# Optimization experiments

Hardware: AMD Instinct MI355X
Metric: run time of the kernel (lower is better)

The kernel has to match this reference:

```python
import jax, jax.numpy as jnp
import numpy as np

B, L, D_MODEL = 2, 2048, 1024
D_STATE, D_CONV, EXPAND, DT_RANK = 16, 4, 2, 64
D_INNER = EXPAND * D_MODEL


def setup_inputs() -> dict:
    key = jax.random.key(0)
    ks = jax.random.split(key, 12)
    s = 0.02
    A_log = jnp.log(jnp.broadcast_to(jnp.arange(1, D_STATE + 1, dtype=jnp.float32), (D_INNER, D_STATE)))
    return {
        "x": jax.random.normal(ks[0], (B, L, D_MODEL), jnp.float32),
        "W_in": jax.random.normal(ks[1], (2 * D_INNER, D_MODEL), jnp.float32) * s,
        "conv_w": jax.random.normal(ks[2], (D_INNER, 1, D_CONV), jnp.float32) * 0.2,
        "conv_b": jax.random.normal(ks[3], (D_INNER,), jnp.float32) * s,
        "W_xp": jax.random.normal(ks[4], (DT_RANK + 2 * D_STATE, D_INNER), jnp.float32) * s,
        "W_dt": jax.random.normal(ks[5], (D_INNER, DT_RANK), jnp.float32) * 0.1,
        "b_dt": jax.random.uniform(ks[6], (D_INNER,), jnp.float32, -4.6, -2.3),  # ~softplus^-1 of small dt
        "A_log": A_log,
        "D": jnp.ones((D_INNER,), jnp.float32),
        "W_out_ssm": jax.random.normal(ks[7], (D_MODEL, D_INNER), jnp.float32) * s,
        "W_out": jax.random.normal(ks[8], (D_MODEL, D_MODEL), jnp.float32) * s,
        "b_out": jnp.zeros((D_MODEL,), jnp.float32),
    }


def _mamba_block(x, W_in, conv_w, conv_b, W_xp, W_dt, b_dt, A_log, D, W_out_ssm, W_out, b_out):
    d_inner = conv_b.shape[0]
    d_state = A_log.shape[1]
    dt_rank = W_dt.shape[1]
    d_conv = conv_w.shape[-1]

    # in_proj -> x branch and gate z
    xz = x @ W_in.T                         # [B, L, 2*d_inner]
    xin, z = jnp.split(xz, 2, axis=-1)

    # causal depthwise conv over time
    xc = jnp.transpose(xin, (0, 2, 1))      # [B, d_inner, L]
    xc = jax.lax.conv_general_dilated(
        xc, conv_w, window_strides=(1,), padding=[(d_conv - 1, 0)],
        feature_group_count=d_inner)
    xc = jax.nn.silu(xc + conv_b[None, :, None])
    xs = jnp.transpose(xc, (0, 2, 1))       # [B, L, d_inner]

    # input-dependent dt, B, C
    x_dbl = xs @ W_xp.T                     # [B, L, dt_rank + 2*d_state]
    dt, Bm, Cm = jnp.split(x_dbl, [dt_rank, dt_rank + d_state], axis=-1)
    dt = jax.nn.softplus(dt @ W_dt.T + b_dt)  # [B, L, d_inner]

    A = -jnp.exp(A_log)                     # [d_inner, d_state]

    def step(h, inp):
        dt_t, B_t, C_t, x_t = inp           # [B,di] [B,ds] [B,ds] [B,di]
        dA = jnp.exp(dt_t[:, :, None] * A)                      # [B, di, ds]
        h = h * dA + (dt_t * x_t)[:, :, None] * B_t[:, None, :]  # [B, di, ds]
        y = jnp.einsum('bds,bs->bd', h, C_t)
        return h, y

    h0 = jnp.zeros((x.shape[0], d_inner, d_state), x.dtype)
    tm = lambda a: jnp.swapaxes(a, 0, 1)    # time-major
    _, ys = jax.lax.scan(step, h0, (tm(dt), tm(Bm), tm(Cm), tm(xs)))
    y = jnp.swapaxes(ys, 0, 1)              # [B, L, d_inner]

    y = y + xs * D
    y = y * jax.nn.silu(z)
    y = y @ W_out_ssm.T                     # mamba-internal out_proj -> d_model
    return y @ W_out.T + b_out              # wrapper out_proj


def reference(x, W_in, conv_w, conv_b, W_xp, W_dt, b_dt, A_log, D, W_out_ssm, W_out, b_out):
    return _mamba_block(x, W_in, conv_w, conv_b, W_xp, W_dt, b_dt, A_log, D, W_out_ssm, W_out, b_out)
```

## Files before the change

kernel.cpp:

```cpp
#include <hip/hip_runtime.h>
#include <hip/hip_bf16.h>
#include <cmath>
#include <cstdint>

typedef __bf16 bf16_t;
typedef bf16_t bf16x8 __attribute__((ext_vector_type(8)));
typedef bf16_t bf16x4 __attribute__((ext_vector_type(4)));
typedef float f32x4 __attribute__((ext_vector_type(4)));

#define BB 2
#define LL 2048
#define DMODEL 1024
#define DINNER 2048
#define DSTATE 16
#define NC 64
#define CHUNK 32
#define KSEG 256

#define EXP2F(x) __builtin_amdgcn_exp2f(x)

#define CVT_N0 1048576
#define CVT_N1 2097152
#define CVT_N2 2129920
#define CVT_N3 2392064
#define CVT_NB0 9344
#define CVT_NB1 10368
#define CVT_NBT 10880
__global__ __launch_bounds__(256) void k_cvt_all(
    const float* __restrict__ x, const float* __restrict__ Win,
    const float* __restrict__ Wdt, const float* __restrict__ Wo,
    const float* __restrict__ Wxp, const float* __restrict__ Wos,
    bf16_t* __restrict__ x_b, bf16_t* __restrict__ Win_b,
    bf16_t* __restrict__ Wdt_b, bf16_t* __restrict__ Wo_b,
    bf16_t* __restrict__ Wxp_b, bf16_t* __restrict__ WosT_b) {
    const int tid = threadIdx.x;
    if (blockIdx.x < CVT_NB0) {
        int i = blockIdx.x * 256 + tid;
        const float* src; bf16_t* dst; int j;
        if (i < CVT_N0)      { src = x;   dst = x_b;   j = i; }
        else if (i < CVT_N1) { src = Win; dst = Win_b; j = i - CVT_N0; }
        else if (i < CVT_N2) { src = Wdt; dst = Wdt_b; j = i - CVT_N1; }
        else                 { src = Wo;  dst = Wo_b;  j = i - CVT_N2; }
        float4 v = reinterpret_cast<const float4*>(src)[j];
        bf16x4 o;
        o[0] = (bf16_t)v.x; o[1] = (bf16_t)v.y; o[2] = (bf16_t)v.z; o[3] = (bf16_t)v.w;
        reinterpret_cast<bf16x4*>(dst)[j] = o;
    } else if (blockIdx.x < CVT_NB1) {
        int i = (blockIdx.x - CVT_NB0) * 256 + tid;
        int r = i >> 11, c = i & (DINNER - 1);
        float v = (r < 96) ? Wxp[r * DINNER + c] : 0.f;
        Wxp_b[i] = (bf16_t)v;
    } else {
        __shared__ float tile[64][65];
        const int bid = blockIdx.x - CVT_NB1;
        const int m0 = (bid & 15) * 64;
        const int d0 = (bid >> 4) * 64;
        const int dl = tid & 63;
        #pragma unroll 4
        for (int i = 0; i < 16; ++i) {
            const int mr = (tid >> 6) + i * 4;
            tile[dl][mr] = Wos[(size_t)(m0 + mr) * DINNER + d0 + dl];
        }
        __syncthreads();
        const int dr = tid >> 2;
        const int q  = tid & 3;
        bf16_t* op = WosT_b + (size_t)(d0 + dr) * DMODEL + m0 + q * 16;
        bf16x8 v0, v1;
        #pragma unroll
        for (int j = 0; j < 8; ++j) v0[j] = (bf16_t)tile[dr][q * 16 + j];
        #pragma unroll
        for (int j = 0; j < 8; ++j) v1[j] = (bf16_t)tile[dr][q * 16 + 8 + j];
        reinterpret_cast<bf16x8*>(op)[0] = v0;
        reinterpret_cast<bf16x8*>(op)[1] = v1;
    }
}

__device__ __forceinline__ void gload16(const void* g, void* l) {
    __builtin_amdgcn_global_load_lds(
        (const __attribute__((address_space(1))) void*)g,
        (__attribute__((address_space(3))) void*)l,
        16, 0, 0);
}

__global__ __launch_bounds__(512) void k_gemm256(
    const bf16_t* __restrict__ x_b, const bf16_t* __restrict__ Win_b,
    bf16_t* __restrict__ xin_b, bf16_t* __restrict__ zsT) {
    __shared__ bf16_t lds[65536];
    const int tid = threadIdx.x;
    const int wid = tid >> 6, lane = tid & 63;

    const int bid = (blockIdx.x & 7) * 32 + (blockIdx.x >> 3);
    const bf16_t* A; const bf16_t* Bt; int m0, n0, sub;
    if (bid < 128) {
        sub = 0; A = x_b; Bt = Win_b;
        m0 = (bid >> 3) * 256; n0 = (bid & 7) * 256;
    } else {
        sub = 1; A = Win_b + (size_t)DINNER * DMODEL; Bt = x_b;
        const int t2 = bid - 128;
        m0 = (t2 >> 4) * 256; n0 = (t2 & 15) * 256;
    }
    const int wr = wid >> 2, wc = wid & 3;
    f32x4 acc[8][4] = {};

    const int srow = tid >> 3;
    const int k8p = (tid & 7) ^ (srow & 7);
    const bf16_t* apA = A + (size_t)(m0 + srow) * 1024 + k8p * 8;
    const bf16_t* apB = Bt + (size_t)(n0 + srow) * 1024 + k8p * 8;

    auto stageA = [&](int slot, int kt) {
        char* b0 = (char*)lds + slot * 32768 + wid * 1024;
        const bf16_t* src = apA + kt * 64;
        gload16(src, b0);
        gload16(src + (size_t)64 * 1024, b0 + 8192);
        gload16(src + (size_t)128 * 1024, b0 + 16384);
        gload16(src + (size_t)192 * 1024, b0 + 24576);
    };
    auto stageB = [&](int slot, int kt) {
        char* b0 = (char*)lds + 65536 + slot * 32768 + wid * 1024;
        const bf16_t* src = apB + kt * 64;
        gload16(src, b0);
        gload16(src + (size_t)64 * 1024, b0 + 8192);
        gload16(src + (size_t)128 * 1024, b0 + 16384);
        gload16(src + (size_t)192 * 1024, b0 + 24576);
    };

    const int lm = lane & 15, lq = lane >> 4;

    const bf16_t* pA0[8]; const bf16_t* pA1[8];
    const bf16_t* pB0[4]; const bf16_t* pB1[4];
    #pragma unroll
    for (int i = 0; i < 8; ++i) {
        const int rr = lm + i * 16;
        const int e0 = wr * 8192 + rr * 64 + (lq ^ (rr & 7)) * 8;
        pA0[i] = lds + e0;
        pA1[i] = lds + (e0 ^ 32);
    }
    #pragma unroll
    for (int j = 0; j < 4; ++j) {
        const int rr = (wc & 1) * 64 + lm + j * 16;
        const int e0 = 32768 + (wc >> 1) * 8192 + rr * 64 + (lq ^ (rr & 7)) * 8;
        pB0[j] = lds + e0;
        pB1[j] = lds + (e0 ^ 32);
    }

    auto body = [&](int t, int s) {
        asm volatile("s_waitcnt vmcnt(0)" ::: "memory");
        __builtin_amdgcn_sched_barrier(0);
        __builtin_amdgcn_s_barrier();
        __builtin_amdgcn_sched_barrier(0);
        if (t + 1 < 16) {
            stageA(s ^ 1, t + 1);
            stageB(s ^ 1, t + 1);
        }
        {
            bf16x8 fa[8], fb[4];
            #pragma unroll
            for (int i = 0; i < 8; ++i) fa[i] = *(const bf16x8*)(pA0[i] + s * 16384);
            #pragma unroll
            for (int j = 0; j < 4; ++j) fb[j] = *(const bf16x8*)(pB0[j] + s * 16384);
            __builtin_amdgcn_s_setprio(1);
            #pragma unroll
            for (int i = 0; i < 8; ++i)
                #pragma unroll
                for (int j = 0; j < 4; ++j)
                    acc[i][j] = __builtin_amdgcn_mfma_f32_16x16x32_bf16(fa[i], fb[j], acc[i][j], 0, 0, 0);
            __builtin_amdgcn_s_setprio(0);
        }
        {
            bf16x8 fa[8], fb[4];
            #pragma unroll
            for (int i = 0; i < 8; ++i) fa[i] = *(const bf16x8*)(pA1[i] + s * 16384);
            #pragma unroll
            for (int j = 0; j < 4; ++j) fb[j] = *(const bf16x8*)(pB1[j] + s * 16384);
            __builtin_amdgcn_s_setprio(1);
            #pragma unroll
            for (int i = 0; i < 8; ++i)
                #pragma unroll
                for (int j = 0; j < 4; ++j)
                    acc[i][j] = __builtin_amdgcn_mfma_f32_16x16x32_bf16(fa[i], fb[j], acc[i][j], 0, 0, 0);
            __builtin_amdgcn_s_setprio(0);
        }
    };

    stageA(0, 0);
    stageB(0, 0);
    for (int tt = 0; tt < 8; ++tt) {
        body(2 * tt, 0);
        body(2 * tt + 1, 1);
    }

    const int row0 = m0 + wr * 128 + lq * 4;
    const int col0 = n0 + wc * 64 + lm;
    #pragma unroll
    for (int i = 0; i < 8; ++i) {
        #pragma unroll
        for (int j = 0; j < 4; ++j) {
            #pragma unroll
            for (int r = 0; r < 4; ++r) {
                const int row = row0 + i * 16 + r;
                const int c = col0 + j * 16;
                float v = acc[i][j][r];
                if (sub == 0) xin_b[(size_t)row * DINNER + c] = (bf16_t)v;
                else          zsT[(size_t)row * (BB * LL) + c] = (bf16_t)(v / (1.f + __expf(-v)));
            }
        }
    }
}

enum { EPI_BF16 = 0, EPI_BIAS = 1, EPI_SOFTPLUS_RB = 3, EPI_PARTK = 4 };

template <int EPI>
__global__ __launch_bounds__(512) void k_gemm_bt(
    const bf16_t* __restrict__ A, const bf16_t* __restrict__ Bt,
    int M, int N, int Kloop, int lda, int ldb,
    float* __restrict__ C, bf16_t* __restrict__ Cb,
    const float* __restrict__ bias,
    float* __restrict__ o_part) {
    __shared__ bf16_t sA[2][128 * 32];
    __shared__ bf16_t sB[2][128 * 32];
    const int tid = threadIdx.x;
    const int wid = tid >> 6, lane = tid & 63;
    const int bx = (blockIdx.x & 7) * ((int)gridDim.x >> 3) + (blockIdx.x >> 3);
    int m0, n0, k0 = 0, seg = 0;
    if (EPI == EPI_PARTK) {
        m0 = (bx & 31) << 7;
        n0 = 0;
        seg = bx >> 5;
        k0 = seg * KSEG;
    } else {
        const int ntile = N >> 7;
        m0 = (bx / ntile) << 7;
        n0 = (bx % ntile) << 7;
    }
    const int wr = wid >> 2, wc = wid & 3;
    f32x4 acc[4][2] = {};

    const bf16_t* ap = A + (size_t)(m0 + (tid >> 2)) * lda + (tid & 3) * 8 + k0;
    const bf16_t* bp = Bt + (size_t)(n0 + (tid >> 2)) * ldb + (tid & 3) * 8 + k0;
    const int lm = lane & 15, lk = (lane >> 4) * 8;

    auto stage = [&](int buf, int kt) {
        char* dA = (char*)sA[buf] + wid * 1024;
        char* dB = (char*)sB[buf] + wid * 1024;
        gload16(ap + kt, dA);
        gload16(bp + kt, dB);
    };

    stage(0, 0);
    __syncthreads();
    int cur = 0;
    for (int kt = 0; kt < Kloop; kt += 32) {
        if (kt + 32 < Kloop) stage(cur ^ 1, kt + 32);
        const bf16_t* rA = sA[cur] + (wr * 64 + lm) * 32 + lk;
        const bf16_t* rB = sB[cur] + (wc * 32 + lm) * 32 + lk;
        bf16x8 fa[4], fb[2];
        #pragma unroll
        for (int i = 0; i < 4; ++i) fa[i] = *(const bf16x8*)(rA + i * 16 * 32);
        #pragma unroll
        for (int j = 0; j < 2; ++j) fb[j] = *(const bf16x8*)(rB + j * 16 * 32);
        __builtin_amdgcn_s_setprio(1);
        #pragma unroll
        for (int i = 0; i < 4; ++i)
            #pragma unroll
            for (int j = 0; j < 2; ++j)
                acc[i][j] = __builtin_amdgcn_mfma_f32_16x16x32_bf16(fa[i], fb[j], acc[i][j], 0, 0, 0);
        __builtin_amdgcn_s_setprio(0);
        __syncthreads();
        cur ^= 1;
    }

    const int row0 = m0 + wr * 64 + (lane >> 4) * 4;
    const int col0 = n0 + wc * 32 + lm;
    float* Cp = (EPI == EPI_PARTK)
        ? o_part + (size_t)seg * ((size_t)4096 * 128)
        : C;
    #pragma unroll
    for (int i = 0; i < 4; ++i) {
        #pragma unroll
        for (int j = 0; j < 2; ++j) {
            #pragma unroll
            for (int r = 0; r < 4; ++r) {
                int row = row0 + i * 16 + r;
                int c = col0 + j * 16;
                float v = acc[i][j][r];
                if (EPI == EPI_BF16) {
                    Cb[(size_t)row * N + c] = (bf16_t)v;
                } else if (EPI == EPI_BIAS) {
                    C[(size_t)row * N + c] = v + bias[c];
                } else if (EPI == EPI_SOFTPLUS_RB) {
                    float xv = v + bias[row];
                    float sp = fmaxf(xv, 0.f) + log1pf(__expf(-fabsf(xv)));
                    Cb[(size_t)row * N + c] = (bf16_t)sp;
                } else {
                    Cp[(size_t)row * 128 + c] = v;
                }
            }
        }
    }
}

__global__ __launch_bounds__(256) void k_split_reduce(
    const float* __restrict__ part, bf16_t* __restrict__ dtr,
    float* __restrict__ Bmf, float* __restrict__ Cmf) {
    int idx = blockIdx.x * 256 + threadIdx.x;
    int row = idx >> 7, c = idx & 127;
    float s = 0.f;
    #pragma unroll
    for (int g = 0; g < 8; ++g) s += part[(size_t)g * (4096 * 128) + idx];
    if (c < 64) dtr[(size_t)row * 64 + c] = (bf16_t)s;
    else if (c < 80) Bmf[(size_t)row * 16 + (c - 64)] = s;
    else if (c < 96) Cmf[(size_t)row * 16 + (c - 80)] = s;
}

__global__ __launch_bounds__(256) void k_conv(
    const bf16_t* __restrict__ xin, const float* __restrict__ cw,
    const float* __restrict__ cb, bf16_t* __restrict__ xs_b,
    bf16_t* __restrict__ xsT) {
    __shared__ float tile[64][65];
    const int tid = threadIdx.x;
    const int d0  = (blockIdx.x & 31) * 64;
    const int bl0 = (blockIdx.x >> 5) * 64;
    const int dl = tid & 63;
    const int d  = d0 + dl;
    const float w0 = cw[d * 4], w1 = cw[d * 4 + 1], w2 = cw[d * 4 + 2], w3 = cw[d * 4 + 3];
    const float bias = cb[d];
    const int l0 = bl0 & (LL - 1);
    #pragma unroll 4
    for (int i = 0; i < 16; ++i) {
        const int blr = (tid >> 6) + i * 4;
        const int bl = bl0 + blr;
        const int l  = l0 + blr;
        const bf16_t* rp = xin + (size_t)bl * DINNER + d;
        float acc = fmaf(w3, (float)rp[0], bias);
        if (l >= 1) acc = fmaf(w2, (float)rp[-(int)DINNER], acc);
        if (l >= 2) acc = fmaf(w1, (float)rp[-2 * (int)DINNER], acc);
        if (l >= 3) acc = fmaf(w0, (float)rp[-3 * (int)DINNER], acc);
        float sv = acc / (1.f + __expf(-acc));
        xs_b[(size_t)bl * DINNER + d] = (bf16_t)sv;
        tile[dl][blr] = sv;
    }
    __syncthreads();
    const int dr = tid >> 2;
    const int q  = tid & 3;
    bf16_t* op = xsT + (size_t)(d0 + dr) * (BB * LL) + bl0 + q * 16;
    bf16x8 v0, v1;
    #pragma unroll
    for (int j = 0; j < 8; ++j) v0[j] = (bf16_t)tile[dr][q * 16 + j];
    #pragma unroll
    for (int j = 0; j < 8; ++j) v1[j] = (bf16_t)tile[dr][q * 16 + 8 + j];
    reinterpret_cast<bf16x8*>(op)[0] = v0;
    reinterpret_cast<bf16x8*>(op)[1] = v1;
}


__global__ __launch_bounds__(256) void k_scan_p1(
    const bf16_t* __restrict__ dtT, const bf16_t* __restrict__ xsT,
    const float* __restrict__ Bm, const float* __restrict__ A_log,
    float* __restrict__ alpha, float* __restrict__ beta) {
    __shared__ float sB[CHUNK * 16];
    const int db = blockIdx.x & 7;
    const int ck = (blockIdx.x >> 3) & (NC - 1);
    const int b  = blockIdx.x >> 9;
    const int tid = threadIdx.x;
    const int d  = db * 256 + tid;
    const int t0 = ck * CHUNK;

    const float* Bsrc = Bm + ((size_t)b * LL + t0) * 16;
    sB[tid] = Bsrc[tid];
    sB[tid + 256] = Bsrc[tid + 256];

    f32x4 a2[4];
    #pragma unroll
    for (int q = 0; q < 4; ++q) {
        f32x4 av = reinterpret_cast<const f32x4*>(A_log + d * 16)[q];
        #pragma unroll
        for (int j = 0; j < 4; ++j) a2[q][j] = -__expf(av[j]) * 1.44269504f;
    }
    const bf16x8* dtp = reinterpret_cast<const bf16x8*>(dtT + (size_t)d * (BB * LL) + b * LL + t0);
    const bf16x8* xsp = reinterpret_cast<const bf16x8*>(xsT + (size_t)d * (BB * LL) + b * LL + t0);

    bf16x8 dtl[4], xsl[4];
    #pragma unroll
    for (int q = 0; q < 4; ++q) dtl[q] = dtp[q];
    #pragma unroll
    for (int q = 0; q < 4; ++q) xsl[q] = xsp[q];

    __syncthreads();

    float al[16], be[16];
    #pragma unroll
    for (int s = 0; s < 16; ++s) { al[s] = 1.f; be[s] = 0.f; }

    #pragma unroll
    for (int t = 0; t < CHUNK; ++t) {
        float dtv = (float)dtl[t >> 3][t & 7];
        float xv  = (float)xsl[t >> 3][t & 7];
        float dtx = dtv * xv;
        #pragma unroll
        for (int q = 0; q < 4; ++q) {
            f32x4 Bq = *reinterpret_cast<const f32x4*>(sB + t * 16 + q * 4);
            #pragma unroll
            for (int j = 0; j < 4; ++j) {
                const int s = q * 4 + j;
                float dA = EXP2F(dtv * a2[q][j]);
                al[s] *= dA;
                be[s] = fmaf(be[s], dA, dtx * Bq[j]);
            }
        }
    }
    float* ap = alpha + ((size_t)(b * NC + ck)) * (DINNER * 16) + (size_t)d * 16;
    float* bp = beta  + ((size_t)(b * NC + ck)) * (DINNER * 16) + (size_t)d * 16;
    #pragma unroll
    for (int q = 0; q < 4; ++q) {
        f32x4 av, bv;
        #pragma unroll
        for (int j = 0; j < 4; ++j) { av[j] = al[q * 4 + j]; bv[j] = be[q * 4 + j]; }
        reinterpret_cast<f32x4*>(ap)[q] = av;
        reinterpret_cast<f32x4*>(bp)[q] = bv;
    }
}

__global__ __launch_bounds__(256) void k_scan_p2(
    const float* __restrict__ alpha, const float* __restrict__ beta,
    float* __restrict__ H) {
    const int gid = blockIdx.x * 256 + threadIdx.x;
    const int b = gid >> 15, r = gid & 32767;
    float h = 0.f;
    #pragma unroll 8
    for (int ck = 0; ck < NC; ++ck) {
        const size_t i = ((size_t)(b * NC + ck)) * 32768 + r;
        H[i] = h;
        h = fmaf(alpha[i], h, beta[i]);
    }
}

__global__ __launch_bounds__(256) void k_scan_p3(
    const bf16_t* __restrict__ dtT, const bf16_t* __restrict__ xsT,
    const float* __restrict__ Bm, const float* __restrict__ Cm,
    const bf16_t* __restrict__ zsT, const float* __restrict__ A_log,
    const float* __restrict__ Dp, const float* __restrict__ H,
    bf16_t* __restrict__ y) {
    __shared__ float sB[CHUNK * 16];
    __shared__ float sC[CHUNK * 16];
    const int db = blockIdx.x & 7;
    const int ck = (blockIdx.x >> 3) & (NC - 1);
    const int b  = blockIdx.x >> 9;
    const int tid = threadIdx.x;
    const int d  = db * 256 + tid;
    const int t0 = ck * CHUNK;

    const float* Bsrc = Bm + ((size_t)b * LL + t0) * 16;
    const float* Csrc = Cm + ((size_t)b * LL + t0) * 16;
    sB[tid] = Bsrc[tid];
    sB[tid + 256] = Bsrc[tid + 256];
    sC[tid] = Csrc[tid];
    sC[tid + 256] = Csrc[tid + 256];

    f32x4 a2[4];
    #pragma unroll
    for (int q = 0; q < 4; ++q) {
        f32x4 av = reinterpret_cast<const f32x4*>(A_log + d * 16)[q];
        #pragma unroll
        for (int j = 0; j < 4; ++j) a2[q][j] = -__expf(av[j]) * 1.44269504f;
    }
    const float Dd = Dp[d];
    const bf16x8* dtp = reinterpret_cast<const bf16x8*>(dtT + (size_t)d * (BB * LL) + b * LL + t0);
    const bf16x8* xsp = reinterpret_cast<const bf16x8*>(xsT + (size_t)d * (BB * LL) + b * LL + t0);
    const bf16x8* zp  = reinterpret_cast<const bf16x8*>(zsT + (size_t)d * (BB * LL) + b * LL + t0);
    bf16_t* yp = y + ((size_t)b * LL + t0) * DINNER + d;

    bf16x8 dtl[4], xsl[4], zsl[4];
    #pragma unroll
    for (int q = 0; q < 4; ++q) dtl[q] = dtp[q];
    #pragma unroll
    for (int q = 0; q < 4; ++q) xsl[q] = xsp[q];
    #pragma unroll
    for (int q = 0; q < 4; ++q) zsl[q] = zp[q];

    float h[16];
    {
        const f32x4* hp = reinterpret_cast<const f32x4*>(H + ((size_t)(b * NC + ck)) * 32768 + (size_t)d * 16);
        #pragma unroll
        for (int q = 0; q < 4; ++q) {
            f32x4 hv = hp[q];
            #pragma unroll
            for (int j = 0; j < 4; ++j) h[q * 4 + j] = hv[j];
        }
    }

    __syncthreads();

    #pragma unroll
    for (int t = 0; t < CHUNK; ++t) {
        float dtv = (float)dtl[t >> 3][t & 7];
        float xv  = (float)xsl[t >> 3][t & 7];
        float zv  = (float)zsl[t >> 3][t & 7];
        float dtx = dtv * xv;
        float yacc = 0.f;
        #pragma unroll
        for (int q = 0; q < 4; ++q) {
            f32x4 Bq = *reinterpret_cast<const f32x4*>(sB + t * 16 + q * 4);
            f32x4 Cq = *reinterpret_cast<const f32x4*>(sC + t * 16 + q * 4);
            #pragma unroll
            for (int j = 0; j < 4; ++j) {
                const int s = q * 4 + j;
                float dA = EXP2F(dtv * a2[q][j]);
                h[s] = fmaf(h[s], dA, dtx * Bq[j]);
                yacc = fmaf(h[s], Cq[j], yacc);
            }
        }
        float yv = (yacc + xv * Dd) * zv;
        yp[(size_t)t * DINNER] = (bf16_t)yv;
    }
}

extern "C" void kernel_launch(void* const* d_in, const int* in_sizes, int n_in,
                              void* d_out, int out_size, void* d_ws, size_t ws_size,
                              hipStream_t stream) {
    const float* x      = (const float*)d_in[0];
    const float* W_in   = (const float*)d_in[1];
    const float* conv_w = (const float*)d_in[2];
    const float* conv_b = (const float*)d_in[3];
    const float* W_xp   = (const float*)d_in[4];
    const float* W_dt   = (const float*)d_in[5];
    const float* b_dt   = (const float*)d_in[6];
    const float* A_log  = (const float*)d_in[7];
    const float* Dvec   = (const float*)d_in[8];
    const float* W_os   = (const float*)d_in[9];
    const float* W_o    = (const float*)d_in[10];
    const float* b_o    = (const float*)d_in[11];
    float* out = (float*)d_out;

    char* base = (char*)d_ws;
    size_t off = 0;
    auto alloc = [&](size_t bytes) -> char* {
        char* p = base + off;
        off += (bytes + 255) & ~(size_t)255;
        return p;
    };
    const int MR = BB * LL;
    bf16_t* x_b   = (bf16_t*)alloc((size_t)MR * DMODEL * 2);
    bf16_t* Win_b = (bf16_t*)alloc((size_t)4096 * 1024 * 2);
    bf16_t* xin_b = (bf16_t*)alloc((size_t)MR * DINNER * 2);
    bf16_t* xs_b  = (bf16_t*)alloc((size_t)MR * DINNER * 2);
    bf16_t* zsT   = (bf16_t*)alloc((size_t)DINNER * MR * 2);
    bf16_t* xsT   = (bf16_t*)alloc((size_t)DINNER * MR * 2);
    bf16_t* dtT_b = (bf16_t*)alloc((size_t)DINNER * MR * 2);
    float*  Hbuf  = (float*)alloc((size_t)BB * NC * DINNER * 16 * 4);
    bf16_t* y_b   = (bf16_t*)alloc((size_t)MR * DINNER * 2);
    bf16_t* dtr_b = (bf16_t*)alloc((size_t)MR * 64 * 2);
    float*  Bmf   = (float*)alloc((size_t)MR * 16 * 4);
    float*  Cmf   = (float*)alloc((size_t)MR * 16 * 4);
    bf16_t* Wxp_b = (bf16_t*)alloc((size_t)128 * DINNER * 2);
    bf16_t* Wdt_b = (bf16_t*)alloc((size_t)DINNER * 64 * 2);
    bf16_t* WosT_b= (bf16_t*)alloc((size_t)DINNER * DMODEL * 2);
    bf16_t* Wo_b  = (bf16_t*)alloc((size_t)DMODEL * DMODEL * 2);
    bf16_t* Wc_b  = (bf16_t*)alloc((size_t)DMODEL * DINNER * 2);

    float* alphab = (float*)xin_b;
    float* betab  = (float*)x_b;
    float* partk  = Hbuf;

    k_cvt_all<<<CVT_NBT, 256, 0, stream>>>(
        x, W_in, W_dt, W_o, W_xp, W_os,
        x_b, Win_b, Wdt_b, Wo_b, Wxp_b, WosT_b);

    k_gemm_bt<EPI_BF16><<<(DMODEL / 128) * (DINNER / 128), 512, 0, stream>>>(
        Wo_b, WosT_b, DMODEL, DINNER, DMODEL, DMODEL, DMODEL,
        nullptr, Wc_b, nullptr, nullptr);
    k_gemm256<<<256, 512, 0, stream>>>(x_b, Win_b, xin_b, zsT);
    k_conv<<<(MR / 64) * (DINNER / 64), 256, 0, stream>>>(xin_b, conv_w, conv_b, xs_b, xsT);
    k_gemm_bt<EPI_PARTK><<<8 * 32, 512, 0, stream>>>(
        xs_b, Wxp_b, MR, 128, KSEG, DINNER, DINNER,
        nullptr, nullptr, nullptr, partk);
    k_split_reduce<<<(MR * 128) / 256, 256, 0, stream>>>(partk, dtr_b, Bmf, Cmf);
    k_gemm_bt<EPI_SOFTPLUS_RB><<<(DINNER / 128) * (MR / 128), 512, 0, stream>>>(
        Wdt_b, dtr_b, DINNER, MR, 64, 64, 64,
        nullptr, dtT_b, b_dt, nullptr);
    k_scan_p1<<<BB * NC * (DINNER / 256), 256, 0, stream>>>(dtT_b, xsT, Bmf, A_log, alphab, betab);
    k_scan_p2<<<(BB * DINNER * DSTATE) / 256, 256, 0, stream>>>(alphab, betab, Hbuf);
    k_scan_p3<<<BB * NC * (DINNER / 256), 256, 0, stream>>>(dtT_b, xsT, Bmf, Cmf, zsT, A_log, Dvec, Hbuf, y_b);
    k_gemm_bt<EPI_BIAS><<<(MR / 128) * (DMODEL / 128), 512, 0, stream>>>(
        y_b, Wc_b, MR, DMODEL, DINNER, DINNER, DINNER,
        out, nullptr, b_o, nullptr);
}
```

Measured before the change: 240.5 us.

## Add async-LDS 128x128 GEMM for weight fold/out-proj and store scan state in bf16

Adds a new 128x128-tile bf16 GEMM kernel that uses direct global-to-LDS loads (gload16), XOR-swizzled LDS, K=64 double buffering and s_setprio around the MFMA blocks. It replaces the older GEMM for the W_out·W_out_ssm weight fold and for the final output projection, aiming to cut load latency and LDS bank conflicts. Separately, the chunked-scan intermediates (alpha, beta, chunk-start H) are now stored in bf16 instead of fp32, halving their memory traffic. The bf16 state carries accuracy risk, because errors in the recurrence can accumulate across chunks.

```diff
diff --git a/kernel.cpp b/kernel.cpp
--- a/kernel.cpp
+++ b/kernel.cpp
@@ -210,6 +210,123 @@
 enum { EPI_BF16 = 0, EPI_BIAS = 1, EPI_SOFTPLUS_RB = 3, EPI_PARTK = 4 };
 
 template <int EPI>
+__global__ __launch_bounds__(512) void k_gemm_cd128(
+    const bf16_t* __restrict__ A, const bf16_t* __restrict__ Bt,
+    int N, int Ktiles, int lda, int ldb,
+    float* __restrict__ C, bf16_t* __restrict__ Cb,
+    const float* __restrict__ bias) {
+    __shared__ bf16_t lds[32768];
+    const int tid = threadIdx.x;
+    const int wid = tid >> 6, lane = tid & 63;
+    const int bx = (blockIdx.x & 7) * ((int)gridDim.x >> 3) + (blockIdx.x >> 3);
+    const int ntile = N >> 7;
+    const int m0 = (bx / ntile) << 7;
+    const int n0 = (bx % ntile) << 7;
+    const int wr = wid >> 2, wc = wid & 3;
+    f32x4 acc[4][2] = {};
+
+    const int srow = tid >> 3;
+    const int k8p = (tid & 7) ^ (srow & 7);
+    const bf16_t* apA = A + (size_t)(m0 + srow) * lda + k8p * 8;
+    const bf16_t* apB = Bt + (size_t)(n0 + srow) * ldb + k8p * 8;
+
+    auto stageA = [&](int slot, int kt) {
+        char* b0 = (char*)lds + slot * 16384 + wid * 1024;
+        const bf16_t* src = apA + kt * 64;
+        gload16(src, b0);
+        gload16(src + (size_t)64 * lda, b0 + 8192);
+    };
+    auto stageB = [&](int slot, int kt) {
+        char* b0 = (char*)lds + 32768 + slot * 16384 + wid * 1024;
+        const bf16_t* src = apB + kt * 64;
+        gload16(src, b0);
+        gload16(src + (size_t)64 * ldb, b0 + 8192);
+    };
+
+    const int lm = lane & 15, lq = lane >> 4;
+
+    const bf16_t* pA0[4]; const bf16_t* pA1[4];
+    const bf16_t* pB0[2]; const bf16_t* pB1[2];
+    #pragma unroll
+    for (int i = 0; i < 4; ++i) {
+        const int rr = lm + i * 16;
+        const int e0 = wr * 4096 + rr * 64 + (lq ^ (rr & 7)) * 8;
+        pA0[i] = lds + e0;
+        pA1[i] = lds + (e0 ^ 32);
+    }
+    #pragma unroll
+    for (int j = 0; j < 2; ++j) {
+        const int rr = wc * 32 + lm + j * 16;
+        const int e0 = 16384 + rr * 64 + (lq ^ (rr & 7)) * 8;
+        pB0[j] = lds + e0;
+        pB1[j] = lds + (e0 ^ 32);
+    }
+
+    auto body = [&](int t, int s) {
+        asm volatile("s_waitcnt vmcnt(0)" ::: "memory");
+        __builtin_amdgcn_sched_barrier(0);
+        __builtin_amdgcn_s_barrier();
+        __builtin_amdgcn_sched_barrier(0);
+        if (t + 1 < Ktiles) {
+            stageA(s ^ 1, t + 1);
+            stageB(s ^ 1, t + 1);
+        }
+        {
+            bf16x8 fa[4], fb[2];
+            #pragma unroll
+            for (int i = 0; i < 4; ++i) fa[i] = *(const bf16x8*)(pA0[i] + s * 8192);
+            #pragma unroll
+            for (int j = 0; j < 2; ++j) fb[j] = *(const bf16x8*)(pB0[j] + s * 8192);
+            __builtin_amdgcn_s_setprio(1);
+            #pragma unroll
+            for (int i = 0; i < 4; ++i)
+                #pragma unroll
+                for (int j = 0; j < 2; ++j)
+                    acc[i][j] = __builtin_amdgcn_mfma_f32_16x16x32_bf16(fa[i], fb[j], acc[i][j], 0, 0, 0);
+            __builtin_amdgcn_s_setprio(0);
+        }
+        {
+            bf16x8 fa[4], fb[2];
+            #pragma unroll
+            for (int i = 0; i < 4; ++i) fa[i] = *(const bf16x8*)(pA1[i] + s * 8192);
+            #pragma unroll
+            for (int j = 0; j < 2; ++j) fb[j] = *(const bf16x8*)(pB1[j] + s * 8192);
+            __builtin_amdgcn_s_setprio(1);
+            #pragma unroll
+            for (int i = 0; i < 4; ++i)
+                #pragma unroll
+                for (int j = 0; j < 2; ++j)
+                    acc[i][j] = __builtin_amdgcn_mfma_f32_16x16x32_bf16(fa[i], fb[j], acc[i][j], 0, 0, 0);
+            __builtin_amdgcn_s_setprio(0);
+        }
+    };
+
+    stageA(0, 0);
+    stageB(0, 0);
+    for (int tt = 0; tt < (Ktiles >> 1); ++tt) {
+        body(2 * tt, 0);
+        body(2 * tt + 1, 1);
+    }
+
+    const int row0 = m0 + wr * 64 + lq * 4;
+    const int col0 = n0 + wc * 32 + lm;
+    #pragma unroll
+    for (int i = 0; i < 4; ++i) {
+        #pragma unroll
+        for (int j = 0; j < 2; ++j) {
+            #pragma unroll
+            for (int r = 0; r < 4; ++r) {
+                const int row = row0 + i * 16 + r;
+                const int c = col0 + j * 16;
+                float v = acc[i][j][r];
+                if (EPI == EPI_BF16) Cb[(size_t)row * N + c] = (bf16_t)v;
+                else                 C[(size_t)row * N + c] = v + bias[c];
+            }
+        }
+    }
+}
+
+template <int EPI>
 __global__ __launch_bounds__(512) void k_gemm_bt(
     const bf16_t* __restrict__ A, const bf16_t* __restrict__ Bt,
     int M, int N, int Kloop, int lda, int ldb,
@@ -283,11 +400,7 @@
                 int row = row0 + i * 16 + r;
                 int c = col0 + j * 16;
                 float v = acc[i][j][r];
-                if (EPI == EPI_BF16) {
-                    Cb[(size_t)row * N + c] = (bf16_t)v;
-                } else if (EPI == EPI_BIAS) {
-                    C[(size_t)row * N + c] = v + bias[c];
-                } else if (EPI == EPI_SOFTPLUS_RB) {
+                if (EPI == EPI_SOFTPLUS_RB) {
                     float xv = v + bias[row];
                     float sp = fmaxf(xv, 0.f) + log1pf(__expf(-fabsf(xv)));
                     Cb[(size_t)row * N + c] = (bf16_t)sp;
@@ -356,7 +469,7 @@
 __global__ __launch_bounds__(256) void k_scan_p1(
     const bf16_t* __restrict__ dtT, const bf16_t* __restrict__ xsT,
     const float* __restrict__ Bm, const float* __restrict__ A_log,
-    float* __restrict__ alpha, float* __restrict__ beta) {
+    bf16_t* __restrict__ alpha, bf16_t* __restrict__ beta) {
     __shared__ float sB[CHUNK * 16];
     const int db = blockIdx.x & 7;
     const int ck = (blockIdx.x >> 3) & (NC - 1);
@@ -408,29 +521,31 @@
             }
         }
     }
-    float* ap = alpha + ((size_t)(b * NC + ck)) * (DINNER * 16) + (size_t)d * 16;
-    float* bp = beta  + ((size_t)(b * NC + ck)) * (DINNER * 16) + (size_t)d * 16;
-    #pragma unroll
-    for (int q = 0; q < 4; ++q) {
-        f32x4 av, bv;
-        #pragma unroll
-        for (int j = 0; j < 4; ++j) { av[j] = al[q * 4 + j]; bv[j] = be[q * 4 + j]; }
-        reinterpret_cast<f32x4*>(ap)[q] = av;
-        reinterpret_cast<f32x4*>(bp)[q] = bv;
-    }
+    bf16_t* ap = alpha + ((size_t)(b * NC + ck)) * (DINNER * 16) + (size_t)d * 16;
+    bf16_t* bp = beta  + ((size_t)(b * NC + ck)) * (DINNER * 16) + (size_t)d * 16;
+    bf16x8 av0, av1, bv0, bv1;
+    #pragma unroll
+    for (int j = 0; j < 8; ++j) {
+        av0[j] = (bf16_t)al[j];     av1[j] = (bf16_t)al[8 + j];
+        bv0[j] = (bf16_t)be[j];     bv1[j] = (bf16_t)be[8 + j];
+    }
+    reinterpret_cast<bf16x8*>(ap)[0] = av0;
+    reinterpret_cast<bf16x8*>(ap)[1] = av1;
+    reinterpret_cast<bf16x8*>(bp)[0] = bv0;
+    reinterpret_cast<bf16x8*>(bp)[1] = bv1;
 }
 
 __global__ __launch_bounds__(256) void k_scan_p2(
-    const float* __restrict__ alpha, const float* __restrict__ beta,
-    float* __restrict__ H) {
+    const bf16_t* __restrict__ alpha, const bf16_t* __restrict__ beta,
+    bf16_t* __restrict__ H) {
     const int gid = blockIdx.x * 256 + threadIdx.x;
     const int b = gid >> 15, r = gid & 32767;
     float h = 0.f;
     #pragma unroll 8
     for (int ck = 0; ck < NC; ++ck) {
         const size_t i = ((size_t)(b * NC + ck)) * 32768 + r;
-        H[i] = h;
-        h = fmaf(alpha[i], h, beta[i]);
+        H[i] = (bf16_t)h;
+        h = fmaf((float)alpha[i], h, (float)beta[i]);
     }
 }
 
@@ -438,7 +553,7 @@
     const bf16_t* __restrict__ dtT, const bf16_t* __restrict__ xsT,
     const float* __restrict__ Bm, const float* __restrict__ Cm,
     const bf16_t* __restrict__ zsT, const float* __restrict__ A_log,
-    const float* __restrict__ Dp, const float* __restrict__ H,
+    const float* __restrict__ Dp, const bf16_t* __restrict__ H,
     bf16_t* __restrict__ y) {
     __shared__ float sB[CHUNK * 16];
     __shared__ float sC[CHUNK * 16];
@@ -479,13 +594,10 @@
 
     float h[16];
     {
-        const f32x4* hp = reinterpret_cast<const f32x4*>(H + ((size_t)(b * NC + ck)) * 32768 + (size_t)d * 16);
-        #pragma unroll
-        for (int q = 0; q < 4; ++q) {
-            f32x4 hv = hp[q];
-            #pragma unroll
-            for (int j = 0; j < 4; ++j) h[q * 4 + j] = hv[j];
-        }
+        const bf16x8* hp = reinterpret_cast<const bf16x8*>(H + ((size_t)(b * NC + ck)) * 32768 + (size_t)d * 16);
+        bf16x8 h0 = hp[0], h1 = hp[1];
+        #pragma unroll
+        for (int j = 0; j < 8; ++j) { h[j] = (float)h0[j]; h[8 + j] = (float)h1[j]; }
     }
 
     __syncthreads();
@@ -557,17 +669,17 @@
     bf16_t* Wo_b  = (bf16_t*)alloc((size_t)DMODEL * DMODEL * 2);
     bf16_t* Wc_b  = (bf16_t*)alloc((size_t)DMODEL * DINNER * 2);
 
-    float* alphab = (float*)xin_b;
-    float* betab  = (float*)x_b;
-    float* partk  = Hbuf;
+    bf16_t* alphab = (bf16_t*)xin_b;
+    bf16_t* betab  = (bf16_t*)x_b;
+    float*  partk  = Hbuf;
+    bf16_t* Hb     = (bf16_t*)Hbuf;
 
     k_cvt_all<<<CVT_NBT, 256, 0, stream>>>(
         x, W_in, W_dt, W_o, W_xp, W_os,
         x_b, Win_b, Wdt_b, Wo_b, Wxp_b, WosT_b);
 
-    k_gemm_bt<EPI_BF16><<<(DMODEL / 128) * (DINNER / 128), 512, 0, stream>>>(
-        Wo_b, WosT_b, DMODEL, DINNER, DMODEL, DMODEL, DMODEL,
-        nullptr, Wc_b, nullptr, nullptr);
+    k_gemm_cd128<EPI_BF16><<<(DMODEL / 128) * (DINNER / 128), 512, 0, stream>>>(
+        Wo_b, WosT_b, DINNER, 16, DMODEL, DMODEL, nullptr, Wc_b, nullptr);
     k_gemm256<<<256, 512, 0, stream>>>(x_b, Win_b, xin_b, zsT);
     k_conv<<<(MR / 64) * (DINNER / 64), 256, 0, stream>>>(xin_b, conv_w, conv_b, xs_b, xsT);
     k_gemm_bt<EPI_PARTK><<<8 * 32, 512, 0, stream>>>(
@@ -578,9 +690,8 @@
         Wdt_b, dtr_b, DINNER, MR, 64, 64, 64,
         nullptr, dtT_b, b_dt, nullptr);
     k_scan_p1<<<BB * NC * (DINNER / 256), 256, 0, stream>>>(dtT_b, xsT, Bmf, A_log, alphab, betab);
-    k_scan_p2<<<(BB * DINNER * DSTATE) / 256, 256, 0, stream>>>(alphab, betab, Hbuf);
-    k_scan_p3<<<BB * NC * (DINNER / 256), 256, 0, stream>>>(dtT_b, xsT, Bmf, Cmf, zsT, A_log, Dvec, Hbuf, y_b);
-    k_gemm_bt<EPI_BIAS><<<(MR / 128) * (DMODEL / 128), 512, 0, stream>>>(
-        y_b, Wc_b, MR, DMODEL, DINNER, DINNER, DINNER,
-        out, nullptr, b_o, nullptr);
-}
+    k_scan_p2<<<(BB * DINNER * DSTATE) / 256, 256, 0, stream>>>(alphab, betab, Hb);
+    k_scan_p3<<<BB * NC * (DINNER / 256), 256, 0, stream>>>(dtT_b, xsT, Bmf, Cmf, zsT, A_log, Dvec, Hb, y_b);
+    k_gemm_cd128<EPI_BIAS><<<(MR / 128) * (DMODEL / 128), 512, 0, stream>>>(
+        y_b, Wc_b, DMODEL, 32, DINNER, DINNER, out, nullptr, b_o);
+}
```

New measurement: 221.0 us, median of 2. -8.1%, faster.
